# Performance work log

Measured on AMD Instinct MI355X. Metric: run time of the kernel, lower is better.

Reference implementation:

```python
import jax, jax.numpy as jnp
import numpy as np
import math
from jax import lax

# cfg['MODEL'] constants
MU = 0.1          # FISTA step size
LMBD = 0.1        # LAMBDA[0], sparsity weight
N_DICT = 1        # EXPANSION_FACTOR
N_STEPS = 6       # NUM_LAYERS (FISTA iterations)
K = 3             # kernel_size
PAD = 1           # padding
STRIDE = 1        # stride (POOLING=False, stride passed to conv)
DN = ('NCHW', 'OIHW', 'NCHW')


def _conv(x, w):
    # F.conv2d(x, w, stride=1, padding=PAD)
    return lax.conv_general_dilated(x, w, (STRIDE, STRIDE), [(PAD, PAD), (PAD, PAD)], dimension_numbers=DN)


def _conv_t(y, w):
    # F.conv_transpose2d(y, w, stride=1, padding=PAD) == conv2d with flipped, in/out-swapped kernel, pad K-1-PAD
    wt = jnp.transpose(jnp.flip(w, (-1, -2)), (1, 0, 2, 3))  # [Cin, Cout, K, K]
    p = K - 1 - PAD
    return lax.conv_general_dilated(y, wt, (1, 1), [(p, p), (p, p)], dimension_numbers=DN)


def _shrink(z, thr):
    # non_negative=True soft-threshold: relu(z - thr)
    return jax.nn.relu(z - thr)


def setup_inputs() -> dict:
    key = jax.random.key(0)
    k1, k2 = jax.random.split(key)
    x = jax.random.normal(k1, (16, 64, 56, 56), dtype=jnp.float32)
    # dictionary weight [out_channels, in_channels*n_dict, K, K], kaiming-ish scale
    W = jax.random.normal(k2, (128, 64 * N_DICT, K, K), dtype=jnp.float32) * 0.05
    return {"x": x, "W": W}


def reference(x, W):
    # w_norm: each output filter normalized to unit Frobenius norm
    Wn = W / jnp.sqrt(jnp.sum(W * W, axis=(1, 2, 3), keepdims=True) + 1e-12)
    thr = MU * LMBD
    xr = jnp.tile(x, (1, N_DICT, 1, 1)) if N_DICT > 1 else x

    # FISTA iteration 0: c = shrink(mu * D^T x)
    c = _shrink(MU * _conv(xr, Wn), thr)
    y = c
    c_prev = c
    t = 1.0
    for _ in range(N_STEPS - 1):
        r = xr - _conv_t(y, Wn)                       # residual x - D c
        c_new = _shrink(y + MU * _conv(r, Wn), thr)   # gradient step + shrink
        t_next = (1.0 + math.sqrt(1.0 + 4.0 * t * t)) / 2.0
        y = c_new + ((t - 1.0) / t_next) * (c_new - c_prev)  # momentum
        c_prev = c_new
        t = t_next
    # POOLING=False -> DictConv2d returns the sparse code directly
    return c_prev
```

## Files before the change

### kernel.cpp

```cpp
#include <hip/hip_runtime.h>
#include <hip/hip_bf16.h>
#include <math.h>

typedef __attribute__((ext_vector_type(8))) short short8;
typedef __attribute__((ext_vector_type(4))) float f32x4;

#define MU_  0.1f
#define THR_ 0.01f

static __device__ inline short f2bf(float f) {
    __hip_bfloat16 h = __float2bfloat16(f);
    return *reinterpret_cast<short*>(&h);
}
static __device__ inline float bf2f(unsigned short u) {
    unsigned int x = ((unsigned int)u) << 16;
    return __builtin_bit_cast(float, x);
}

__global__ __launch_bounds__(256) void zero_kernel(float4* p, int n4) {
    int i = blockIdx.x * 256 + threadIdx.x;
    if (i < n4) p[i] = make_float4(0.f, 0.f, 0.f, 0.f);
}

__global__ __launch_bounds__(64) void wnorm_pack(
    const float* __restrict__ W, short* __restrict__ Wf2, short* __restrict__ Wt2) {
    int co = blockIdx.x, ci = threadIdx.x;
    const float* wp = W + (co * 64 + ci) * 9;
    float v[9]; float s = 0.f;
#pragma unroll
    for (int t = 0; t < 9; ++t) { v[t] = wp[t]; s += v[t] * v[t]; }
#pragma unroll
    for (int off = 32; off; off >>= 1) s += __shfl_xor(s, off, 64);
    float inv = 1.0f / sqrtf(s + 1e-12f);
#pragma unroll
    for (int t = 0; t < 9; ++t) {
        Wf2[((t * 8 + (ci >> 3)) * 128 + co) * 8 + (ci & 7)] = f2bf(v[t] * inv);
        Wt2[((t * 16 + (co >> 3)) * 64 + ci) * 8 + (co & 7)] = f2bf(v[8 - t] * inv);
    }
}

__global__ __launch_bounds__(256) void pack_x(
    const float* __restrict__ x, short* __restrict__ Xp) {
    __shared__ float lx[64 * 57];
    int row = blockIdx.x, n = blockIdx.y, tid = threadIdx.x;
    short* dst = Xp + ((size_t)(n * 58 + row) * 68) * 64;
    if (row >= 1 && row <= 56) {
        int h = row - 1;
        for (int j = tid; j < 64 * 56; j += 256) {
            int ci = j / 56, w = j - ci * 56;
            lx[ci * 57 + w] = x[((size_t)(n * 64 + ci)) * 3136 + h * 56 + w];
        }
        __syncthreads();
        for (int j = tid; j < 68 * 64; j += 256) {
            int s = j >> 6, ci = j & 63;
            float val = (s >= 2 && s < 58) ? lx[ci * 57 + (s - 2)] : 0.f;
            dst[(s << 6) + (ci ^ ((s & 7) << 3))] = f2bf(val);
        }
    } else {
        for (int j = tid; j < 68 * 64; j += 256) dst[j] = 0;
    }
}

__global__ __launch_bounds__(256) void conv_fwd(
    const short* __restrict__ inp,
    const short* __restrict__ Wf2,
    short* __restrict__ Yp,
    short* __restrict__ Cp,
    float* __restrict__ outp, int mode, float beta) {
    __shared__ __align__(16) short smem[14688];
    const int r = blockIdx.x + 1, cb = blockIdx.y, n = blockIdx.z, tid = threadIdx.x;
    {
        const short8* src = (const short8*)(inp + ((size_t)(n * 58 + (r - 1)) * 68) * 64);
        for (int j = tid; j < 1632; j += 256) {
            int srow = j >> 3, w = j & 7;
            *(short8*)(smem + srow * 72 + w * 8) = src[j];
        }
    }
    const int lane = tid & 63, ct = tid >> 6, quad = lane >> 4, l15 = lane & 15;
    const int co = cb * 64 + ct * 16 + l15;

    short8 Areg[18];
#pragma unroll
    for (int f = 0; f < 18; ++f) {
        int t = f >> 1, half = f & 1;
        Areg[f] = *(const short8*)(Wf2 + ((size_t)((t * 8 + half * 4 + quad) * 128 + co)) * 8);
    }
    __syncthreads();

    f32x4 acc[4];
#pragma unroll
    for (int pt = 0; pt < 4; ++pt) acc[pt] = (f32x4){0.f, 0.f, 0.f, 0.f};

#pragma unroll
    for (int f = 0; f < 18; ++f) {
        const int t = f >> 1, half = f & 1;
        const int dh = t / 3, dw = t % 3;
        const int u = l15 + dw + 1;
        const int phys = (half * 4 + quad) ^ (u & 7);
        const int base = (dh * 68 + u) * 72 + phys * 8;
#pragma unroll
        for (int pt = 0; pt < 4; ++pt) {
            short8 bv = *(const short8*)(smem + base + pt * 1152);
            acc[pt] = __builtin_amdgcn_mfma_f32_16x16x32_bf16(Areg[f], bv, acc[pt], 0, 0, 0);
        }
    }

    __syncthreads();
    short* tb_y = smem;
    short* tb_c = smem + 4608;
    const size_t prow = ((size_t)(n * 58 + r) * 68) * 128;
    if (mode != 0) {
        for (int item = tid; item < 448; item += 256) {
            int vv = item >> 3, g = item & 7;
            int s = vv + 2;
            size_t off = prow + (size_t)s * 128 + 8 * ((g + 8 * cb) ^ (s & 7));
            int o = vv * 72 + 8 * (g ^ (vv & 3));
            *(short8*)(tb_y + o) = *(const short8*)(Yp + off);
            if (mode == 1) *(short8*)(tb_c + o) = *(const short8*)(Cp + off);
        }
    }
    __syncthreads();
    const int h = r - 1;
#pragma unroll
    for (int pt = 0; pt < 4; ++pt) {
        const int px = pt * 16 + l15;
#pragma unroll
        for (int reg = 0; reg < 4; ++reg) {
            const int lch = ct * 16 + quad * 4 + reg;
            const int slot = px * 72 + (lch ^ ((px & 3) << 3));
            const float a = acc[pt][reg];
            if (mode == 0) {
                float c = fmaxf(MU_ * a - THR_, 0.f);
                short cb16 = f2bf(c);
                tb_y[slot] = cb16;
                tb_c[slot] = cb16;
            } else if (mode == 1) {
                float yold = bf2f((unsigned short)tb_y[slot]);
                float cold = bf2f((unsigned short)tb_c[slot]);
                float c = fmaxf(yold + MU_ * a - THR_, 0.f);
                tb_y[slot] = f2bf(c + beta * (c - cold));
                tb_c[slot] = f2bf(c);
            } else {
                if (px < 56) {
                    float yold = bf2f((unsigned short)tb_y[slot]);
                    float c = fmaxf(yold + MU_ * a - THR_, 0.f);
                    outp[((size_t)(n * 128 + cb * 64 + lch)) * 3136 + h * 56 + px] = c;
                }
            }
        }
    }
    if (mode != 2) {
        __syncthreads();
        for (int item = tid; item < 448; item += 256) {
            int vv = item >> 3, g = item & 7;
            int so = vv * 72 + 8 * (g ^ (vv & 3));
            short8 yv = *(const short8*)(tb_y + so);
            short8 cv = *(const short8*)(tb_c + so);
            int s = vv + 2;
            size_t off = prow + (size_t)s * 128 + 8 * ((g + 8 * cb) ^ (s & 7));
            *(short8*)(Yp + off) = yv;
            *(short8*)(Cp + off) = cv;
        }
    }
}

__global__ __launch_bounds__(256) void conv_t(
    const short* __restrict__ Ypb,
    const short* __restrict__ Wt2,
    const short* __restrict__ Xp,
    short* __restrict__ Rp) {
    __shared__ __align__(16) short smem[14688];
    const int r = blockIdx.x + 1, n = blockIdx.y, tid = threadIdx.x;
    const int lane = tid & 63, ct = tid >> 6, quad = lane >> 4, l15 = lane & 15;
    const int ci = ct * 16 + l15;
    const short8* src = (const short8*)(Ypb + ((size_t)(n * 58 + (r - 1)) * 68) * 128);

    f32x4 acc[4];
#pragma unroll
    for (int pt = 0; pt < 4; ++pt) acc[pt] = (f32x4){0.f, 0.f, 0.f, 0.f};

#pragma unroll
    for (int p = 0; p < 2; ++p) {
        if (p) __syncthreads();
        for (int j = tid; j < 1632; j += 256) {
            int srow = j >> 3, w = j & 7;
            *(short8*)(smem + srow * 72 + w * 8) = src[srow * 16 + p * 8 + w];
        }
        short8 Areg[18];
#pragma unroll
        for (int f = 0; f < 18; ++f) {
            int t = f >> 1, sh = f & 1;
            Areg[f] = *(const short8*)(Wt2 +
                ((size_t)((t * 16 + (p * 2 + sh) * 4 + quad) * 64 + ci)) * 8);
        }
        __syncthreads();
#pragma unroll
        for (int f = 0; f < 18; ++f) {
            const int t = f >> 1, sh = f & 1;
            const int dh = t / 3, dw = t % 3;
            const int u = l15 + dw + 1;
            const int phys = (sh * 4 + quad) ^ (u & 7);
            const int base = (dh * 68 + u) * 72 + phys * 8;
#pragma unroll
            for (int pt = 0; pt < 4; ++pt) {
                short8 bv = *(const short8*)(smem + base + pt * 1152);
                acc[pt] = __builtin_amdgcn_mfma_f32_16x16x32_bf16(Areg[f], bv, acc[pt], 0, 0, 0);
            }
        }
    }

    __syncthreads();
    short* tb = smem;
    const size_t prow = ((size_t)(n * 58 + r) * 68) * 64;
    for (int item = tid; item < 448; item += 256) {
        int vv = item >> 3, g = item & 7;
        int s = vv + 2;
        *(short8*)(tb + vv * 72 + 8 * (g ^ (vv & 3))) =
            *(const short8*)(Xp + prow + (size_t)s * 64 + 8 * (g ^ (s & 7)));
    }
    __syncthreads();
#pragma unroll
    for (int pt = 0; pt < 4; ++pt) {
        const int px = pt * 16 + l15;
#pragma unroll
        for (int reg = 0; reg < 4; ++reg) {
            const int cir = ct * 16 + quad * 4 + reg;
            const int slot = px * 72 + (cir ^ ((px & 3) << 3));
            float xo = bf2f((unsigned short)tb[slot]);
            tb[slot] = f2bf(xo - acc[pt][reg]);
        }
    }
    __syncthreads();
    for (int item = tid; item < 448; item += 256) {
        int vv = item >> 3, g = item & 7;
        short8 val = *(const short8*)(tb + vv * 72 + 8 * (g ^ (vv & 3)));
        int s = vv + 2;
        *(short8*)(Rp + prow + (size_t)s * 64 + 8 * (g ^ (s & 7))) = val;
    }
}

extern "C" void kernel_launch(void* const* d_in, const int* in_sizes, int n_in,
                              void* d_out, int out_size, void* d_ws, size_t ws_size,
                              hipStream_t stream) {
    const float* x = (const float*)d_in[0];
    const float* W = (const float*)d_in[1];
    float* out = (float*)d_out;

    const size_t XPN = (size_t)16 * 58 * 68 * 64;
    const size_t YPN = 2 * XPN;
    short* Xp = (short*)d_ws;
    short* Rp = Xp + XPN;
    short* Yp = Rp + XPN;
    short* Cp = Yp + YPN;
    short* Wf2 = Cp + YPN;
    short* Wt2 = Wf2 + 73728;

    const int n4 = (int)((XPN + YPN) * 2 / 16);
    hipLaunchKernelGGL(zero_kernel, dim3((n4 + 255) / 256), dim3(256), 0, stream,
                       (float4*)Rp, n4);
    hipLaunchKernelGGL(wnorm_pack, dim3(128), dim3(64), 0, stream, W, Wf2, Wt2);
    hipLaunchKernelGGL(pack_x, dim3(58, 16), dim3(256), 0, stream, x, Xp);

    dim3 gf(56, 2, 16), gt(56, 16), b(256, 1, 1);
    hipLaunchKernelGGL(conv_fwd, gf, b, 0, stream, Xp, Wf2, Yp, Cp,
                       (float*)nullptr, 0, 0.f);
    double t = 1.0;
    for (int it = 1; it <= 5; ++it) {
        hipLaunchKernelGGL(conv_t, gt, b, 0, stream, Yp, Wt2, Xp, Rp);
        double tn = (1.0 + sqrt(1.0 + 4.0 * t * t)) / 2.0;
        float beta = (float)((t - 1.0) / tn);
        hipLaunchKernelGGL(conv_fwd, gf, b, 0, stream, Rp, Wf2, Yp, Cp,
                           (it == 5) ? out : (float*)nullptr, (it == 5) ? 2 : 1,
                           beta);
        t = tn;
    }
}
```

Baseline: 372.4 us.

## Fuse prep kernels, prefetch epilogue loads, split weight registers, remap blocks

Merges the zeroing, weight-normalization and input-packing kernels into one launch to cut launch overhead. In both conv kernels the epilogue's global loads of old Y/C or X are issued before the MFMA loop so their latency overlaps compute. The per-thread weight fragments are loaded in two halves of nine instead of eighteen, and launch bounds request four blocks per CU, aiming for higher occupancy. Blocks are remapped from 3D to 1D with an interleaved row ordering, presumably to spread work across XCDs for cache locality. Holding the prefetched values in registers across the MMA loop adds register pressure.

```diff
diff --git a/kernel.cpp b/kernel.cpp
--- a/kernel.cpp
+++ b/kernel.cpp
@@ -17,58 +17,66 @@
     return __builtin_bit_cast(float, x);
 }
 
-__global__ __launch_bounds__(256) void zero_kernel(float4* p, int n4) {
-    int i = blockIdx.x * 256 + threadIdx.x;
-    if (i < n4) p[i] = make_float4(0.f, 0.f, 0.f, 0.f);
-}
-
-__global__ __launch_bounds__(64) void wnorm_pack(
-    const float* __restrict__ W, short* __restrict__ Wf2, short* __restrict__ Wt2) {
-    int co = blockIdx.x, ci = threadIdx.x;
-    const float* wp = W + (co * 64 + ci) * 9;
-    float v[9]; float s = 0.f;
-#pragma unroll
-    for (int t = 0; t < 9; ++t) { v[t] = wp[t]; s += v[t] * v[t]; }
-#pragma unroll
-    for (int off = 32; off; off >>= 1) s += __shfl_xor(s, off, 64);
-    float inv = 1.0f / sqrtf(s + 1e-12f);
-#pragma unroll
-    for (int t = 0; t < 9; ++t) {
-        Wf2[((t * 8 + (ci >> 3)) * 128 + co) * 8 + (ci & 7)] = f2bf(v[t] * inv);
-        Wt2[((t * 16 + (co >> 3)) * 64 + ci) * 8 + (co & 7)] = f2bf(v[8 - t] * inv);
-    }
-}
-
-__global__ __launch_bounds__(256) void pack_x(
-    const float* __restrict__ x, short* __restrict__ Xp) {
+#define ZB_ 5916
+
+__global__ __launch_bounds__(256) void prep_kernel(
+    const float* __restrict__ x, const float* __restrict__ W,
+    float4* __restrict__ zbase, int n4,
+    short* __restrict__ Xp, short* __restrict__ Wf2, short* __restrict__ Wt2) {
     __shared__ float lx[64 * 57];
-    int row = blockIdx.x, n = blockIdx.y, tid = threadIdx.x;
-    short* dst = Xp + ((size_t)(n * 58 + row) * 68) * 64;
-    if (row >= 1 && row <= 56) {
-        int h = row - 1;
-        for (int j = tid; j < 64 * 56; j += 256) {
-            int ci = j / 56, w = j - ci * 56;
-            lx[ci * 57 + w] = x[((size_t)(n * 64 + ci)) * 3136 + h * 56 + w];
-        }
-        __syncthreads();
-        for (int j = tid; j < 68 * 64; j += 256) {
-            int s = j >> 6, ci = j & 63;
-            float val = (s >= 2 && s < 58) ? lx[ci * 57 + (s - 2)] : 0.f;
-            dst[(s << 6) + (ci ^ ((s & 7) << 3))] = f2bf(val);
+    const int bid = blockIdx.x, tid = threadIdx.x;
+    if (bid < ZB_) {
+        int i = bid * 256 + tid;
+        if (i < n4) zbase[i] = make_float4(0.f, 0.f, 0.f, 0.f);
+    } else if (bid < ZB_ + 32) {
+        int co = (bid - ZB_) * 4 + (tid >> 6);
+        int ci = tid & 63;
+        const float* wp = W + (co * 64 + ci) * 9;
+        float v[9]; float s = 0.f;
+#pragma unroll
+        for (int t = 0; t < 9; ++t) { v[t] = wp[t]; s += v[t] * v[t]; }
+#pragma unroll
+        for (int off = 32; off; off >>= 1) s += __shfl_xor(s, off, 64);
+        float inv = 1.0f / sqrtf(s + 1e-12f);
+#pragma unroll
+        for (int t = 0; t < 9; ++t) {
+            Wf2[((t * 8 + (ci >> 3)) * 128 + co) * 8 + (ci & 7)] = f2bf(v[t] * inv);
+            Wt2[((t * 16 + (co >> 3)) * 64 + ci) * 8 + (co & 7)] = f2bf(v[8 - t] * inv);
         }
     } else {
-        for (int j = tid; j < 68 * 64; j += 256) dst[j] = 0;
-    }
-}
-
-__global__ __launch_bounds__(256) void conv_fwd(
+        int pb = bid - ZB_ - 32;
+        int row = pb % 58, n = pb / 58;
+        short* dst = Xp + ((size_t)(n * 58 + row) * 68) * 64;
+        if (row >= 1 && row <= 56) {
+            int h = row - 1;
+            for (int j = tid; j < 64 * 56; j += 256) {
+                int ci = j / 56, w = j - ci * 56;
+                lx[ci * 57 + w] = x[((size_t)(n * 64 + ci)) * 3136 + h * 56 + w];
+            }
+            __syncthreads();
+            for (int j = tid; j < 68 * 64; j += 256) {
+                int s = j >> 6, ci = j & 63;
+                float val = (s >= 2 && s < 58) ? lx[ci * 57 + (s - 2)] : 0.f;
+                dst[(s << 6) + (ci ^ ((s & 7) << 3))] = f2bf(val);
+            }
+        } else {
+            for (int j = tid; j < 68 * 64; j += 256) dst[j] = 0;
+        }
+    }
+}
+
+__global__ __launch_bounds__(256, 4) void conv_fwd(
     const short* __restrict__ inp,
     const short* __restrict__ Wf2,
     short* __restrict__ Yp,
     short* __restrict__ Cp,
     float* __restrict__ outp, int mode, float beta) {
     __shared__ __align__(16) short smem[14688];
-    const int r = blockIdx.x + 1, cb = blockIdx.y, n = blockIdx.z, tid = threadIdx.x;
+    const int bid = blockIdx.x, tid = threadIdx.x;
+    const int cb = bid >= 896;
+    const int q = bid - cb * 896;
+    const int sid = (q & 7) * 112 + (q >> 3);
+    const int n = sid / 56, r = sid - n * 56 + 1;
     {
         const short8* src = (const short8*)(inp + ((size_t)(n * 58 + (r - 1)) * 68) * 64);
         for (int j = tid; j < 1632; j += 256) {
@@ -78,12 +86,21 @@
     }
     const int lane = tid & 63, ct = tid >> 6, quad = lane >> 4, l15 = lane & 15;
     const int co = cb * 64 + ct * 16 + l15;
-
-    short8 Areg[18];
-#pragma unroll
-    for (int f = 0; f < 18; ++f) {
-        int t = f >> 1, half = f & 1;
-        Areg[f] = *(const short8*)(Wf2 + ((size_t)((t * 8 + half * 4 + quad) * 128 + co)) * 8);
+    const size_t prow = ((size_t)(n * 58 + r) * 68) * 128;
+
+    short8 yold8[2], cold8[2];
+    int pvv[2], pg[2]; bool pok[2];
+#pragma unroll
+    for (int k = 0; k < 2; ++k) {
+        int item = tid + k * 256;
+        pok[k] = item < 448;
+        pvv[k] = item >> 3; pg[k] = item & 7;
+        if (mode != 0 && pok[k]) {
+            int s = pvv[k] + 2;
+            size_t off = prow + (size_t)s * 128 + 8 * ((pg[k] + 8 * cb) ^ (s & 7));
+            yold8[k] = *(const short8*)(Yp + off);
+            if (mode == 1) cold8[k] = *(const short8*)(Cp + off);
+        }
     }
     __syncthreads();
 
@@ -92,31 +109,38 @@
     for (int pt = 0; pt < 4; ++pt) acc[pt] = (f32x4){0.f, 0.f, 0.f, 0.f};
 
 #pragma unroll
-    for (int f = 0; f < 18; ++f) {
-        const int t = f >> 1, half = f & 1;
-        const int dh = t / 3, dw = t % 3;
-        const int u = l15 + dw + 1;
-        const int phys = (half * 4 + quad) ^ (u & 7);
-        const int base = (dh * 68 + u) * 72 + phys * 8;
-#pragma unroll
-        for (int pt = 0; pt < 4; ++pt) {
-            short8 bv = *(const short8*)(smem + base + pt * 1152);
-            acc[pt] = __builtin_amdgcn_mfma_f32_16x16x32_bf16(Areg[f], bv, acc[pt], 0, 0, 0);
+    for (int hp = 0; hp < 2; ++hp) {
+        short8 Areg[9];
+#pragma unroll
+        for (int i = 0; i < 9; ++i) {
+            int f = hp * 9 + i, t = f >> 1, half = f & 1;
+            Areg[i] = *(const short8*)(Wf2 +
+                ((size_t)((t * 8 + half * 4 + quad) * 128 + co)) * 8);
+        }
+#pragma unroll
+        for (int i = 0; i < 9; ++i) {
+            const int f = hp * 9 + i, t = f >> 1, half = f & 1;
+            const int dh = t / 3, dw = t % 3;
+            const int u = l15 + dw + 1;
+            const int phys = (half * 4 + quad) ^ (u & 7);
+            const int base = (dh * 68 + u) * 72 + phys * 8;
+#pragma unroll
+            for (int pt = 0; pt < 4; ++pt) {
+                short8 bv = *(const short8*)(smem + base + pt * 1152);
+                acc[pt] = __builtin_amdgcn_mfma_f32_16x16x32_bf16(Areg[i], bv, acc[pt], 0, 0, 0);
+            }
         }
     }
 
     __syncthreads();
     short* tb_y = smem;
     short* tb_c = smem + 4608;
-    const size_t prow = ((size_t)(n * 58 + r) * 68) * 128;
     if (mode != 0) {
-        for (int item = tid; item < 448; item += 256) {
-            int vv = item >> 3, g = item & 7;
-            int s = vv + 2;
-            size_t off = prow + (size_t)s * 128 + 8 * ((g + 8 * cb) ^ (s & 7));
-            int o = vv * 72 + 8 * (g ^ (vv & 3));
-            *(short8*)(tb_y + o) = *(const short8*)(Yp + off);
-            if (mode == 1) *(short8*)(tb_c + o) = *(const short8*)(Cp + off);
+#pragma unroll
+        for (int k = 0; k < 2; ++k) if (pok[k]) {
+            int o = pvv[k] * 72 + 8 * (pg[k] ^ (pvv[k] & 3));
+            *(short8*)(tb_y + o) = yold8[k];
+            if (mode == 1) *(short8*)(tb_c + o) = cold8[k];
         }
     }
     __syncthreads();
@@ -164,16 +188,32 @@
     }
 }
 
-__global__ __launch_bounds__(256) void conv_t(
+__global__ __launch_bounds__(256, 4) void conv_t(
     const short* __restrict__ Ypb,
     const short* __restrict__ Wt2,
     const short* __restrict__ Xp,
     short* __restrict__ Rp) {
     __shared__ __align__(16) short smem[14688];
-    const int r = blockIdx.x + 1, n = blockIdx.y, tid = threadIdx.x;
+    const int bid = blockIdx.x, tid = threadIdx.x;
+    const int sid = (bid & 7) * 112 + (bid >> 3);
+    const int n = sid / 56, r = sid - n * 56 + 1;
     const int lane = tid & 63, ct = tid >> 6, quad = lane >> 4, l15 = lane & 15;
     const int ci = ct * 16 + l15;
     const short8* src = (const short8*)(Ypb + ((size_t)(n * 58 + (r - 1)) * 68) * 128);
+    const size_t prow = ((size_t)(n * 58 + r) * 68) * 64;
+
+    short8 xold8[2];
+    int pvv[2], pg[2]; bool pok[2];
+#pragma unroll
+    for (int k = 0; k < 2; ++k) {
+        int item = tid + k * 256;
+        pok[k] = item < 448;
+        pvv[k] = item >> 3; pg[k] = item & 7;
+        if (pok[k]) {
+            int s = pvv[k] + 2;
+            xold8[k] = *(const short8*)(Xp + prow + (size_t)s * 64 + 8 * (pg[k] ^ (s & 7)));
+        }
+    }
 
     f32x4 acc[4];
 #pragma unroll
@@ -186,37 +226,37 @@
             int srow = j >> 3, w = j & 7;
             *(short8*)(smem + srow * 72 + w * 8) = src[srow * 16 + p * 8 + w];
         }
-        short8 Areg[18];
-#pragma unroll
-        for (int f = 0; f < 18; ++f) {
-            int t = f >> 1, sh = f & 1;
-            Areg[f] = *(const short8*)(Wt2 +
-                ((size_t)((t * 16 + (p * 2 + sh) * 4 + quad) * 64 + ci)) * 8);
-        }
         __syncthreads();
 #pragma unroll
-        for (int f = 0; f < 18; ++f) {
-            const int t = f >> 1, sh = f & 1;
-            const int dh = t / 3, dw = t % 3;
-            const int u = l15 + dw + 1;
-            const int phys = (sh * 4 + quad) ^ (u & 7);
-            const int base = (dh * 68 + u) * 72 + phys * 8;
-#pragma unroll
-            for (int pt = 0; pt < 4; ++pt) {
-                short8 bv = *(const short8*)(smem + base + pt * 1152);
-                acc[pt] = __builtin_amdgcn_mfma_f32_16x16x32_bf16(Areg[f], bv, acc[pt], 0, 0, 0);
+        for (int sub = 0; sub < 2; ++sub) {
+            short8 Areg[9];
+#pragma unroll
+            for (int i = 0; i < 9; ++i) {
+                int f = sub * 9 + i, t = f >> 1, sh = f & 1;
+                Areg[i] = *(const short8*)(Wt2 +
+                    ((size_t)((t * 16 + (p * 2 + sh) * 4 + quad) * 64 + ci)) * 8);
+            }
+#pragma unroll
+            for (int i = 0; i < 9; ++i) {
+                const int f = sub * 9 + i, t = f >> 1, sh = f & 1;
+                const int dh = t / 3, dw = t % 3;
+                const int u = l15 + dw + 1;
+                const int phys = (sh * 4 + quad) ^ (u & 7);
+                const int base = (dh * 68 + u) * 72 + phys * 8;
+#pragma unroll
+                for (int pt = 0; pt < 4; ++pt) {
+                    short8 bv = *(const short8*)(smem + base + pt * 1152);
+                    acc[pt] = __builtin_amdgcn_mfma_f32_16x16x32_bf16(Areg[i], bv, acc[pt], 0, 0, 0);
+                }
             }
         }
     }
 
     __syncthreads();
     short* tb = smem;
-    const size_t prow = ((size_t)(n * 58 + r) * 68) * 64;
-    for (int item = tid; item < 448; item += 256) {
-        int vv = item >> 3, g = item & 7;
-        int s = vv + 2;
-        *(short8*)(tb + vv * 72 + 8 * (g ^ (vv & 3))) =
-            *(const short8*)(Xp + prow + (size_t)s * 64 + 8 * (g ^ (s & 7)));
+#pragma unroll
+    for (int k = 0; k < 2; ++k) if (pok[k]) {
+        *(short8*)(tb + pvv[k] * 72 + 8 * (pg[k] ^ (pvv[k] & 3))) = xold8[k];
     }
     __syncthreads();
 #pragma unroll
@@ -256,20 +296,19 @@
     short* Wt2 = Wf2 + 73728;
 
     const int n4 = (int)((XPN + YPN) * 2 / 16);
-    hipLaunchKernelGGL(zero_kernel, dim3((n4 + 255) / 256), dim3(256), 0, stream,
-                       (float4*)Rp, n4);
-    hipLaunchKernelGGL(wnorm_pack, dim3(128), dim3(64), 0, stream, W, Wf2, Wt2);
-    hipLaunchKernelGGL(pack_x, dim3(58, 16), dim3(256), 0, stream, x, Xp);
-
-    dim3 gf(56, 2, 16), gt(56, 16), b(256, 1, 1);
-    hipLaunchKernelGGL(conv_fwd, gf, b, 0, stream, Xp, Wf2, Yp, Cp,
+    const int prep_blocks = ZB_ + 32 + 58 * 16;
+    hipLaunchKernelGGL(prep_kernel, dim3(prep_blocks), dim3(256), 0, stream,
+                       x, W, (float4*)Rp, n4, Xp, Wf2, Wt2);
+
+    dim3 b(256, 1, 1);
+    hipLaunchKernelGGL(conv_fwd, dim3(1792), b, 0, stream, Xp, Wf2, Yp, Cp,
                        (float*)nullptr, 0, 0.f);
     double t = 1.0;
     for (int it = 1; it <= 5; ++it) {
-        hipLaunchKernelGGL(conv_t, gt, b, 0, stream, Yp, Wt2, Xp, Rp);
+        hipLaunchKernelGGL(conv_t, dim3(896), b, 0, stream, Yp, Wt2, Xp, Rp);
         double tn = (1.0 + sqrt(1.0 + 4.0 * t * t)) / 2.0;
         float beta = (float)((t - 1.0) / tn);
-        hipLaunchKernelGGL(conv_fwd, gf, b, 0, stream, Rp, Wf2, Yp, Cp,
+        hipLaunchKernelGGL(conv_fwd, dim3(1792), b, 0, stream, Rp, Wf2, Yp, Cp,
                            (it == 5) ? out : (float*)nullptr, (it == 5) ? 2 : 1,
                            beta);
         t = tn;
```

Measured after the change: 360.5 us. 1.03x faster.
